# Optimization experiments

Hardware: AMD Instinct MI355X
Metric: run time of the kernel (lower is better)

## Reference

```python
import jax, jax.numpy as jnp
import numpy as np

D_MODEL, H, D_FF = 512, 8, 2048
B, S = 2, 2048
EPS = 1e-6


def _layernorm(x, alpha, beta):
    # Faithful to the torch module: unbiased std (ddof=1), eps added to STD,
    # scalar alpha/beta parameters.
    m = jnp.mean(x, axis=-1, keepdims=True)
    var = jnp.sum((x - m) ** 2, axis=-1, keepdims=True) / (x.shape[-1] - 1)
    std = jnp.sqrt(var)
    return alpha * (x - m) / (std + EPS) + beta


def _mha(x, mask, Wq, bq, Wk, bk, Wv, bv, Wo, bo):
    Bn, Sn, D = x.shape
    dk = D // H
    q = (x @ Wq + bq).reshape(Bn, Sn, H, dk).transpose(0, 2, 1, 3)  # [B,H,S,dk]
    k = (x @ Wk + bk).reshape(Bn, Sn, H, dk).transpose(0, 2, 1, 3)
    v = (x @ Wv + bv).reshape(Bn, Sn, H, dk).transpose(0, 2, 1, 3)
    scores = jnp.einsum('bhqd,bhkd->bhqk', q, k) / jnp.sqrt(jnp.float32(dk))
    scores = jnp.where(mask == 0, -jnp.inf, scores)  # mask [B,1,1,S] broadcasts
    attn = jax.nn.softmax(scores, axis=-1)
    out = jnp.einsum('bhqk,bhkd->bhqd', attn, v)
    out = out.transpose(0, 2, 1, 3).reshape(Bn, Sn, D)
    return out @ Wo + bo


def _ffn(x, W1, b1, W2, b2):
    return jax.nn.relu(x @ W1 + b1) @ W2 + b2


def setup_inputs() -> dict:
    key = jax.random.key(0)
    ks = jax.random.split(key, 12)
    sd = 1.0 / np.sqrt(D_MODEL)
    sdf = 1.0 / np.sqrt(D_FF)
    inp = {
        'x': jax.random.normal(ks[0], (B, S, D_MODEL), jnp.float32),
        'src_mask': jnp.ones((B, 1, 1, S), jnp.int32),
        'Wq': jax.random.normal(ks[1], (D_MODEL, D_MODEL), jnp.float32) * sd,
        'bq': jnp.zeros((D_MODEL,), jnp.float32),
        'Wk': jax.random.normal(ks[2], (D_MODEL, D_MODEL), jnp.float32) * sd,
        'bk': jnp.zeros((D_MODEL,), jnp.float32),
        'Wv': jax.random.normal(ks[3], (D_MODEL, D_MODEL), jnp.float32) * sd,
        'bv': jnp.zeros((D_MODEL,), jnp.float32),
        'Wo': jax.random.normal(ks[4], (D_MODEL, D_MODEL), jnp.float32) * sd,
        'bo': jnp.zeros((D_MODEL,), jnp.float32),
        'W1': jax.random.normal(ks[5], (D_MODEL, D_FF), jnp.float32) * sd,
        'b1': jnp.zeros((D_FF,), jnp.float32),
        'W2': jax.random.normal(ks[6], (D_FF, D_MODEL), jnp.float32) * sdf,
        'b2': jnp.zeros((D_MODEL,), jnp.float32),
        'alpha1': jnp.ones((1,), jnp.float32),
        'beta1': jnp.zeros((1,), jnp.float32),
        'alpha2': jnp.ones((1,), jnp.float32),
        'beta2': jnp.zeros((1,), jnp.float32),
    }
    return inp


def reference(x, src_mask, Wq, bq, Wk, bk, Wv, bv, Wo, bo,
              W1, b1, W2, b2, alpha1, beta1, alpha2, beta2):
    # SkipConnection 0: x + dropout(MHA(LN(x)))  (dropout=0 -> identity)
    h1 = _layernorm(x, alpha1, beta1)
    x = x + _mha(h1, src_mask, Wq, bq, Wk, bk, Wv, bv, Wo, bo)
    # SkipConnection 1: x + dropout(FFN(LN(x)))
    h2 = _layernorm(x, alpha2, beta2)
    x = x + _ffn(h2, W1, b1, W2, b2)
    return x
```

## Files before the change

### kernel.cpp

```cpp
#include <hip/hip_runtime.h>
#include <hip/hip_bf16.h>

typedef __hip_bfloat16 bf16;
typedef __attribute__((ext_vector_type(8))) short s8v;
typedef __attribute__((ext_vector_type(4))) float f32x4;

#define DM 512
#define NH 8
#define DKH 64
#define DFF 2048
#define NB 2
#define NS 2048
#define NR (NB*NS)
#define LN_EPS 1e-6f
#define NEG_BIG (-1e30f)
#define LDQKV (3*DM)
#define SM_SHIFT (-6.0f)
#define PART_ELEMS (NB*NH*NS*DKH)

#define MFMA_B16(a,b,c) __builtin_amdgcn_mfma_f32_16x16x32_bf16(a,b,c,0,0,0)

#define GLOAD16(g, l) __builtin_amdgcn_global_load_lds( \
    (const __attribute__((address_space(1))) void*)(g), \
    (__attribute__((address_space(3))) void*)(l), 16, 0, 0)

__device__ __forceinline__ float us2f(unsigned int u){ return __uint_as_float(u << 16); }
__device__ __forceinline__ float b2f(bf16 v){ return __bfloat162float(v); }
__device__ __forceinline__ float ldf(const float* p){ return *p; }
__device__ __forceinline__ float ldf(const bf16* p){ return __bfloat162float(*p); }
__device__ __forceinline__ void stf(float* p, float v){ *p = v; }
__device__ __forceinline__ void stf(bf16* p, float v){ *p = __float2bfloat16(v); }
__device__ __forceinline__ unsigned short f2bu(float f){
  bf16 b = __float2bfloat16(f);
  return *reinterpret_cast<unsigned short*>(&b);
}

template<int N> __device__ __forceinline__ void waitcnt_vm(){
  if constexpr(N==0)      asm volatile("s_waitcnt vmcnt(0)" ::: "memory");
  else if constexpr(N==2) asm volatile("s_waitcnt vmcnt(2)" ::: "memory");
  else if constexpr(N==3) asm volatile("s_waitcnt vmcnt(3)" ::: "memory");
  else if constexpr(N==4) asm volatile("s_waitcnt vmcnt(4)" ::: "memory");
  else if constexpr(N==6) asm volatile("s_waitcnt vmcnt(6)" ::: "memory");
  else if constexpr(N==8) asm volatile("s_waitcnt vmcnt(8)" ::: "memory");
}

__device__ __forceinline__ int swz(int row, int colbyte){
  return ((row<<7) + colbyte) ^ ((row&7)<<4);
}

__device__ __forceinline__ float wsum(float v){
#pragma unroll
  for(int o=32;o>0;o>>=1) v += __shfl_down(v,o,64);
  return v;
}

template<int NTHR>
__device__ __forceinline__ void stage_tile(char* lds, const bf16* g, int ld, int R, int tid){
  int nch = R*8;
  for(int c = tid; c < nch; c += NTHR){
    int row = c>>3;
    int blk = (c&7) ^ (row&7);
    GLOAD16(g + (size_t)row*ld + blk*8, lds + c*16);
  }
}
__device__ __forceinline__ s8v read_frag(const char* lds, int row, int col){
  return *reinterpret_cast<const s8v*>(lds + swz(row, col<<1));
}

template<typename TI>
__global__ __launch_bounds__(256) void ln_kernel(const TI* __restrict__ x,
    bf16* __restrict__ out, const float* __restrict__ ap, const float* __restrict__ bp){
  __shared__ float s1[4], s2[4];
  int row = blockIdx.x, tid = threadIdx.x;
  const TI* xr = x + (size_t)row*DM;
  float v0 = ldf(xr+tid), v1 = ldf(xr+tid+256);
  float s = wsum(v0+v1);
  float q = wsum(v0*v0+v1*v1);
  int wid = tid>>6, lane = tid&63;
  if(lane==0){ s1[wid]=s; s2[wid]=q; }
  __syncthreads();
  float S = s1[0]+s1[1]+s1[2]+s1[3];
  float Q = s2[0]+s2[1]+s2[2]+s2[3];
  float mean = S*(1.f/DM);
  float var  = (Q - (float)DM*mean*mean)*(1.f/(DM-1));
  float sd   = sqrtf(fmaxf(var,0.f));
  float sc = (*ap)/(sd+LN_EPS);
  float b = *bp;
  bf16* orow = out + (size_t)row*DM;
  orow[tid]     = __float2bfloat16((v0-mean)*sc + b);
  orow[tid+256] = __float2bfloat16((v1-mean)*sc + b);
}

__global__ __launch_bounds__(256) void transpose_all(
    const float* __restrict__ Wq, const float* __restrict__ Wk,
    const float* __restrict__ Wv, const float* __restrict__ Wo,
    const float* __restrict__ W1, const float* __restrict__ W2,
    bf16* __restrict__ WTqkv, bf16* __restrict__ WTo,
    bf16* __restrict__ WT1, bf16* __restrict__ WT2){
  __shared__ float t[64][65];
  int tb = blockIdx.x;
  const float* W; bf16* WT; int K, N, nx;
  if(tb < 192){
    int w = tb>>6; tb &= 63;
    W = (w==0)?Wq:(w==1)?Wk:Wv; WT = WTqkv + w*512*512; K=512; N=512; nx=8;
  } else if(tb < 256){ tb -= 192; W=Wo; WT=WTo; K=512; N=512; nx=8; }
  else if(tb < 512){ tb -= 256; W=W1; WT=WT1; K=512; N=2048; nx=32; }
  else { tb -= 512; W=W2; WT=WT2; K=2048; N=512; nx=8; }
  int n0 = (tb % nx)*64, k0 = (tb / nx)*64;
  int tid = threadIdx.x;
  int rr = tid>>6, cc = tid&63;
#pragma unroll
  for(int r=rr;r<64;r+=4) t[r][cc] = W[(size_t)(k0+r)*N + n0+cc];
  __syncthreads();
#pragma unroll
  for(int r=rr;r<64;r+=4) WT[(size_t)(n0+r)*K + k0+cc] = __float2bfloat16(t[cc][r]);
}

__global__ __launch_bounds__(256) void transpose_v(const bf16* __restrict__ Vg,
    bf16* __restrict__ VT){
  __shared__ float t[64][65];
  int tid = threadIdx.x;
  int s0 = blockIdx.x*64; int bh = blockIdx.y;
  int b = bh>>3, h = bh&7;
  int rr = tid>>6, cc = tid&63;
#pragma unroll
  for(int r=rr;r<64;r+=4)
    t[r][cc] = b2f(Vg[((size_t)(b*NS + s0+r))*LDQKV + h*DKH + cc]);
  __syncthreads();
  int kp = (cc&15)*4 + (cc>>4);
#pragma unroll
  for(int r=rr;r<64;r+=4)
    VT[((size_t)bh*DKH + r)*NS + s0 + kp] = __float2bfloat16(t[cc][r]);
}

template<int BM, int BN, int RELU, int QKVSEL, typename TR, typename TO>
__global__ __launch_bounds__(256) void mfma_gemm(
    const bf16* __restrict__ A, const bf16* __restrict__ WT,
    const float* __restrict__ bias0, const float* __restrict__ bias1,
    const float* __restrict__ bias2,
    const TR* __restrict__ resid, TO* __restrict__ out, int M, int N, int K){
  constexpr int NW = BN/2, NF = NW/16, MI = (BM+31)/32, WRS = BM/2;
  constexpr int LOADS = BM/32 + BN/32;
  __shared__ char lA[2][BM*128];
  __shared__ char lB[2][BN*128];
  int tid = threadIdx.x, wave = tid>>6, lane = tid&63;
  int m0 = blockIdx.x*BM, n0 = blockIdx.y*BN;
  int wr = wave>>1, wc = wave&1;
  int g = lane>>4, li = lane&15;
  f32x4 acc[MI][NF] = {};
  stage_tile<256>(lA[0], A + (size_t)m0*K, K, BM, tid);
  stage_tile<256>(lB[0], WT + (size_t)n0*K, K, BN, tid);
  int NT = K>>6;
  int cur = 0;
  for(int t=0; t<NT; ++t, cur^=1){
    if(t+1 < NT){
      stage_tile<256>(lA[cur^1], A + (size_t)m0*K + (t+1)*64, K, BM, tid);
      stage_tile<256>(lB[cur^1], WT + (size_t)n0*K + (t+1)*64, K, BN, tid);
      waitcnt_vm<LOADS>();
    } else {
      waitcnt_vm<0>();
    }
    __builtin_amdgcn_sched_barrier(0);
    __builtin_amdgcn_s_barrier();
    __builtin_amdgcn_sched_barrier(0);
#pragma unroll
    for(int kk=0; kk<2; kk++){
      s8v af[MI], bfr[NF];
#pragma unroll
      for(int mi=0;mi<MI;mi++) af[mi] = read_frag(lA[cur], wr*WRS+mi*16+li, kk*32+g*8);
#pragma unroll
      for(int ni=0;ni<NF;ni++) bfr[ni] = read_frag(lB[cur], wc*NW+ni*16+li, kk*32+g*8);
#pragma unroll
      for(int mi=0;mi<MI;mi++)
#pragma unroll
        for(int ni=0;ni<NF;ni++)
          acc[mi][ni] = MFMA_B16(af[mi], bfr[ni], acc[mi][ni]);
    }
    __builtin_amdgcn_sched_barrier(0);
    __builtin_amdgcn_s_barrier();
  }
#pragma unroll
  for(int mi=0;mi<MI;mi++)
#pragma unroll
  for(int ni=0;ni<NF;ni++){
    int row = m0 + wr*WRS + mi*16 + g*4;
    int col = n0 + wc*NW + ni*16 + li;
    const float* bp = bias0;
    if(QKVSEL) bp = (col<512)? bias0 : (col<1024)? (bias1-512) : (bias2-1024);
    float bb = bp[col];
#pragma unroll
    for(int r=0;r<4;r++){
      float v = acc[mi][ni][r] + bb;
      if(RELU) v = fmaxf(v, 0.f);
      size_t off = (size_t)(row+r)*N + col;
      if(resid) v += ldf(resid+off);
      stf(out+off, v);
    }
  }
}

__global__ __launch_bounds__(512,4) void flash_attn(
    const bf16* __restrict__ QKV, const bf16* __restrict__ VT,
    const int* __restrict__ mask, bf16* __restrict__ partA,
    bf16* __restrict__ partB, float* __restrict__ lbuf){
  __shared__ char lK[2][64*128];
  __shared__ char lV[2][64*128];
  __shared__ char lP[8][16*128];
  int tid = threadIdx.x, wave = tid>>6, lane = tid&63;
  int bid = blockIdx.x;
  int xcd = bid & 7, u = bid >> 3;
  int q0 = (u & 15)*128;
  int bhk = xcd + 8*(u>>4);
  int h = bhk & 7, kh = (bhk>>3)&1, b = bhk>>4;
  int kbase = kh*(NS/2);
  int g = lane>>4, li = lane&15;
  const bf16* Qg  = QKV + ((size_t)b*NS + q0)*LDQKV + h*DKH;
  const bf16* Kg  = QKV + ((size_t)b*NS + kbase)*LDQKV + DM + h*DKH;
  const bf16* VTg = VT + ((size_t)(b*NH + h))*DKH*NS + kbase;
  stage_tile<512>((char*)lK, Qg, LDQKV, 128, tid);
  __syncthreads();
  s8v qf0 = read_frag((char*)lK, wave*16+li, g*8);
  s8v qf1 = read_frag((char*)lK, wave*16+li, 32+g*8);
  __syncthreads();
  stage_tile<512>(lK[0], Kg, LDQKV, 64, tid);
  stage_tile<512>(lV[0], VTg, NS, 64, tid);
  unsigned long long mb = 0;
#pragma unroll 16
  for(int j=0;j<64;j++)
    mb |= (unsigned long long)(mask[b*NS + kbase + j*16 + li] != 0) << j;
  __syncthreads();
  f32x4 acc[4] = {};
  f32x4 acc_l = {};
  s8v ones;
#pragma unroll
  for(int j=0;j<8;j++) ones[j] = (short)0x3F80;
  char* lPw = lP[wave];

  auto compute = [&](int kt, int c){
    f32x4 S[4] = {};
    __builtin_amdgcn_s_setprio(1);
#pragma unroll
    for(int kk=0;kk<2;kk++){
      s8v qf = kk ? qf1 : qf0;
      s8v kf[4];
#pragma unroll
      for(int ni=0;ni<4;ni++) kf[ni] = read_frag(lK[c], ni*16+li, kk*32+g*8);
#pragma unroll
      for(int ni=0;ni<4;ni++)
        S[ni] = MFMA_B16(qf, kf[ni], S[ni]);
    }
    __builtin_amdgcn_s_setprio(0);
    int jb = kt>>4;
    float madd[4];
#pragma unroll
    for(int ni=0;ni<4;ni++)
      madd[ni] = ((mb>>(jb+ni))&1ull) ? SM_SHIFT : NEG_BIG;
#pragma unroll
    for(int r=0;r<4;r++){
      float e0 = __expf(fmaf(S[0][r], 0.125f, madd[0]));
      float e1 = __expf(fmaf(S[1][r], 0.125f, madd[1]));
      float e2 = __expf(fmaf(S[2][r], 0.125f, madd[2]));
      float e3 = __expf(fmaf(S[3][r], 0.125f, madd[3]));
      int row = g*4 + r;
      uint2 w;
      w.x = (unsigned int)f2bu(e0) | ((unsigned int)f2bu(e1)<<16);
      w.y = (unsigned int)f2bu(e2) | ((unsigned int)f2bu(e3)<<16);
      *reinterpret_cast<uint2*>(lPw + swz(row, li<<3)) = w;
    }
    __builtin_amdgcn_s_setprio(1);
#pragma unroll
    for(int kk=0;kk<2;kk++){
      s8v pf = read_frag(lPw, li, kk*32+g*8);
      s8v vf[4];
#pragma unroll
      for(int nd=0;nd<4;nd++) vf[nd] = read_frag(lV[c], nd*16+li, kk*32+g*8);
#pragma unroll
      for(int nd=0;nd<4;nd++)
        acc[nd] = MFMA_B16(pf, vf[nd], acc[nd]);
      acc_l = MFMA_B16(pf, ones, acc_l);
    }
    __builtin_amdgcn_s_setprio(0);
  };

  int cur = 0;
  for(int t=0; t<15; ++t, cur^=1){
    stage_tile<512>(lK[cur^1], Kg + (size_t)(t+1)*64*LDQKV, LDQKV, 64, tid);
    stage_tile<512>(lV[cur^1], VTg + (t+1)*64, NS, 64, tid);
    waitcnt_vm<2>();
    __builtin_amdgcn_sched_barrier(0);
    __builtin_amdgcn_s_barrier();
    __builtin_amdgcn_sched_barrier(0);
    compute(t*64, cur);
    __builtin_amdgcn_sched_barrier(0);
    __builtin_amdgcn_s_barrier();
  }
  waitcnt_vm<0>();
  __builtin_amdgcn_sched_barrier(0);
  __builtin_amdgcn_s_barrier();
  __builtin_amdgcn_sched_barrier(0);
  compute(15*64, cur);

  bf16* part = kh ? partB : partA;
  size_t qb = (size_t)(b*NH + h)*NS;
#pragma unroll
  for(int r=0;r<4;r++){
    int qrow = q0 + wave*16 + g*4 + r;
#pragma unroll
    for(int nd=0;nd<4;nd++)
      part[(qb + qrow)*DKH + nd*16 + li] = __float2bfloat16(acc[nd][r]);
    if(li==0)
      lbuf[((size_t)((b*NH+h)*2 + kh))*NS + qrow] = acc_l[r];
  }
}

__global__ __launch_bounds__(256) void combine_attn(const bf16* __restrict__ pA,
    const bf16* __restrict__ pB, const float* __restrict__ lbuf,
    bf16* __restrict__ cx){
  int e = blockIdx.x*256 + threadIdx.x;
  int idx = e*4;
  int d = idx & 63, q = (idx>>6)&(NS-1), h = (idx>>17)&7, b = idx>>20;
  uint2 ua = *reinterpret_cast<const uint2*>(pA+idx);
  uint2 ub = *reinterpret_cast<const uint2*>(pB+idx);
  float lA = lbuf[((size_t)((b*NH+h)*2+0))*NS + q];
  float lB = lbuf[((size_t)((b*NH+h)*2+1))*NS + q];
  float il = 1.f/(lA+lB);
  bf16* o = cx + ((size_t)(b*NS+q)*DM + h*DKH + d);
  o[0] = __float2bfloat16((us2f(ua.x&0xffffu)+us2f(ub.x&0xffffu))*il);
  o[1] = __float2bfloat16((us2f(ua.x>>16)+us2f(ub.x>>16))*il);
  o[2] = __float2bfloat16((us2f(ua.y&0xffffu)+us2f(ub.y&0xffffu))*il);
  o[3] = __float2bfloat16((us2f(ua.y>>16)+us2f(ub.y>>16))*il);
}

extern "C" void kernel_launch(void* const* d_in, const int* in_sizes, int n_in,
                              void* d_out, int out_size, void* d_ws, size_t ws_size,
                              hipStream_t stream){
  const float* x   = (const float*)d_in[0];
  const int* mask  = (const int*)d_in[1];
  const float* Wq = (const float*)d_in[2];
  const float* bq = (const float*)d_in[3];
  const float* Wk = (const float*)d_in[4];
  const float* bk = (const float*)d_in[5];
  const float* Wv = (const float*)d_in[6];
  const float* bv = (const float*)d_in[7];
  const float* Wo = (const float*)d_in[8];
  const float* bo = (const float*)d_in[9];
  const float* W1 = (const float*)d_in[10];
  const float* b1 = (const float*)d_in[11];
  const float* W2 = (const float*)d_in[12];
  const float* b2 = (const float*)d_in[13];
  const float* a1 = (const float*)d_in[14];
  const float* be1= (const float*)d_in[15];
  const float* a2 = (const float*)d_in[16];
  const float* be2= (const float*)d_in[17];

  char* ws = (char*)d_ws;
  bf16* h1    = (bf16*)(ws);
  bf16* accA  = (bf16*)(ws);
  bf16* WTqkv = (bf16*)(ws + (size_t)( 4<<20));
  bf16* WTo   = (bf16*)(ws + (size_t)(11<<19));
  bf16* WT1   = (bf16*)(ws + (size_t)( 8<<20));
  bf16* WT2   = (bf16*)(ws + (size_t)(10<<20));
  bf16* qkv   = (bf16*)(ws + (size_t)(12<<20));
  bf16* VT    = (bf16*)(ws + (size_t)(24<<20));
  bf16* cx    = (bf16*)(ws + (size_t)(24<<20));
  bf16* x1    = h1;
  bf16* h2    = (bf16*)(ws + (size_t)( 4<<20));
  bf16* mid   = qkv;
  float* lbuf = (float*)d_out;
  bf16* accB  = (bf16*)((char*)d_out + (1<<20));

  transpose_all<<<768,256,0,stream>>>(Wq,Wk,Wv,Wo,W1,W2, WTqkv,WTo,WT1,WT2);

  ln_kernel<float><<<NR,256,0,stream>>>(x, h1, a1, be1);
  mfma_gemm<128,64,0,1,float,bf16><<<dim3(32,24),256,0,stream>>>(
      h1, WTqkv, bq, bk, bv, (const float*)nullptr, qkv, NR, LDQKV, DM);
  transpose_v<<<dim3(32,16),256,0,stream>>>(qkv + 2*DM, VT);
  flash_attn<<<512,512,0,stream>>>(qkv, VT, mask, accA, accB, lbuf);
  combine_attn<<<PART_ELEMS/1024,256,0,stream>>>(accA, accB, lbuf, cx);
  mfma_gemm<32,64,0,0,float,bf16><<<dim3(128,8),256,0,stream>>>(
      cx, WTo, bo, bo, bo, x, x1, NR, DM, DM);
  ln_kernel<bf16><<<NR,256,0,stream>>>(x1, h2, a2, be2);
  mfma_gemm<128,128,1,0,float,bf16><<<dim3(32,16),256,0,stream>>>(
      h2, WT1, b1, b1, b1, (const float*)nullptr, mid, NR, DFF, DM);
  mfma_gemm<32,64,0,0,bf16,float><<<dim3(128,8),256,0,stream>>>(
      mid, WT2, b2, b2, b2, x1, (float*)d_out, NR, DM, DFF);
}
```

Before: 127.1 us.

## Give each attention wave 32 query rows with 256-thread blocks

The flash attention kernel moves from 8 waves handling 16 query rows each to 4 waves handling 32 rows each, so every K and V fragment read from LDS feeds two MFMA row tiles. Blocks shrink to 256 threads, and the staging and wait counts change to match. This halves the LDS fragment reads per MFMA and the number of waves sharing a barrier. The cost is twice the accumulator registers per wave, fewer threads issuing the global-to-LDS loads, and possibly lower occupancy.

```diff
diff --git a/kernel.cpp b/kernel.cpp
--- a/kernel.cpp
+++ b/kernel.cpp
@@ -199,13 +199,13 @@
   }
 }
 
-__global__ __launch_bounds__(512,4) void flash_attn(
+__global__ __launch_bounds__(256,3) void flash_attn(
     const bf16* __restrict__ QKV, const bf16* __restrict__ VT,
     const int* __restrict__ mask, bf16* __restrict__ partA,
     bf16* __restrict__ partB, float* __restrict__ lbuf){
   __shared__ char lK[2][64*128];
   __shared__ char lV[2][64*128];
-  __shared__ char lP[8][16*128];
+  __shared__ char lP[4][32*128];
   int tid = threadIdx.x, wave = tid>>6, lane = tid&63;
   int bid = blockIdx.x;
   int xcd = bid & 7, u = bid >> 3;
@@ -217,37 +217,42 @@
   const bf16* Qg  = QKV + ((size_t)b*NS + q0)*LDQKV + h*DKH;
   const bf16* Kg  = QKV + ((size_t)b*NS + kbase)*LDQKV + DM + h*DKH;
   const bf16* VTg = VT + ((size_t)(b*NH + h))*DKH*NS + kbase;
-  stage_tile<512>((char*)lK, Qg, LDQKV, 128, tid);
-  __syncthreads();
-  s8v qf0 = read_frag((char*)lK, wave*16+li, g*8);
-  s8v qf1 = read_frag((char*)lK, wave*16+li, 32+g*8);
-  __syncthreads();
-  stage_tile<512>(lK[0], Kg, LDQKV, 64, tid);
-  stage_tile<512>(lV[0], VTg, NS, 64, tid);
+  stage_tile<256>((char*)lK, Qg, LDQKV, 128, tid);
+  __syncthreads();
+  s8v qf[2][2];
+#pragma unroll
+  for(int mi=0;mi<2;mi++)
+#pragma unroll
+    for(int kk=0;kk<2;kk++)
+      qf[mi][kk] = read_frag((char*)lK, wave*32+mi*16+li, kk*32+g*8);
+  __syncthreads();
+  stage_tile<256>(lK[0], Kg, LDQKV, 64, tid);
+  stage_tile<256>(lV[0], VTg, NS, 64, tid);
   unsigned long long mb = 0;
 #pragma unroll 16
   for(int j=0;j<64;j++)
     mb |= (unsigned long long)(mask[b*NS + kbase + j*16 + li] != 0) << j;
   __syncthreads();
-  f32x4 acc[4] = {};
-  f32x4 acc_l = {};
+  f32x4 acc[2][4] = {};
+  f32x4 acc_l[2] = {};
   s8v ones;
 #pragma unroll
   for(int j=0;j<8;j++) ones[j] = (short)0x3F80;
   char* lPw = lP[wave];
 
   auto compute = [&](int kt, int c){
-    f32x4 S[4] = {};
+    f32x4 S[2][4] = {};
     __builtin_amdgcn_s_setprio(1);
 #pragma unroll
     for(int kk=0;kk<2;kk++){
-      s8v qf = kk ? qf1 : qf0;
       s8v kf[4];
 #pragma unroll
       for(int ni=0;ni<4;ni++) kf[ni] = read_frag(lK[c], ni*16+li, kk*32+g*8);
 #pragma unroll
-      for(int ni=0;ni<4;ni++)
-        S[ni] = MFMA_B16(qf, kf[ni], S[ni]);
+      for(int mi=0;mi<2;mi++)
+#pragma unroll
+        for(int ni=0;ni<4;ni++)
+          S[mi][ni] = MFMA_B16(qf[mi][kk], kf[ni], S[mi][ni]);
     }
     __builtin_amdgcn_s_setprio(0);
     int jb = kt>>4;
@@ -256,12 +261,14 @@
     for(int ni=0;ni<4;ni++)
       madd[ni] = ((mb>>(jb+ni))&1ull) ? SM_SHIFT : NEG_BIG;
 #pragma unroll
+    for(int mi=0;mi<2;mi++)
+#pragma unroll
     for(int r=0;r<4;r++){
-      float e0 = __expf(fmaf(S[0][r], 0.125f, madd[0]));
-      float e1 = __expf(fmaf(S[1][r], 0.125f, madd[1]));
-      float e2 = __expf(fmaf(S[2][r], 0.125f, madd[2]));
-      float e3 = __expf(fmaf(S[3][r], 0.125f, madd[3]));
-      int row = g*4 + r;
+      float e0 = __expf(fmaf(S[mi][0][r], 0.125f, madd[0]));
+      float e1 = __expf(fmaf(S[mi][1][r], 0.125f, madd[1]));
+      float e2 = __expf(fmaf(S[mi][2][r], 0.125f, madd[2]));
+      float e3 = __expf(fmaf(S[mi][3][r], 0.125f, madd[3]));
+      int row = mi*16 + g*4 + r;
       uint2 w;
       w.x = (unsigned int)f2bu(e0) | ((unsigned int)f2bu(e1)<<16);
       w.y = (unsigned int)f2bu(e2) | ((unsigned int)f2bu(e3)<<16);
@@ -270,23 +277,26 @@
     __builtin_amdgcn_s_setprio(1);
 #pragma unroll
     for(int kk=0;kk<2;kk++){
-      s8v pf = read_frag(lPw, li, kk*32+g*8);
       s8v vf[4];
 #pragma unroll
       for(int nd=0;nd<4;nd++) vf[nd] = read_frag(lV[c], nd*16+li, kk*32+g*8);
 #pragma unroll
-      for(int nd=0;nd<4;nd++)
-        acc[nd] = MFMA_B16(pf, vf[nd], acc[nd]);
-      acc_l = MFMA_B16(pf, ones, acc_l);
+      for(int mi=0;mi<2;mi++){
+        s8v pf = read_frag(lPw, mi*16+li, kk*32+g*8);
+#pragma unroll
+        for(int nd=0;nd<4;nd++)
+          acc[mi][nd] = MFMA_B16(pf, vf[nd], acc[mi][nd]);
+        acc_l[mi] = MFMA_B16(pf, ones, acc_l[mi]);
+      }
     }
     __builtin_amdgcn_s_setprio(0);
   };
 
   int cur = 0;
   for(int t=0; t<15; ++t, cur^=1){
-    stage_tile<512>(lK[cur^1], Kg + (size_t)(t+1)*64*LDQKV, LDQKV, 64, tid);
-    stage_tile<512>(lV[cur^1], VTg + (t+1)*64, NS, 64, tid);
-    waitcnt_vm<2>();
+    stage_tile<256>(lK[cur^1], Kg + (size_t)(t+1)*64*LDQKV, LDQKV, 64, tid);
+    stage_tile<256>(lV[cur^1], VTg + (t+1)*64, NS, 64, tid);
+    waitcnt_vm<4>();
     __builtin_amdgcn_sched_barrier(0);
     __builtin_amdgcn_s_barrier();
     __builtin_amdgcn_sched_barrier(0);
@@ -303,13 +313,15 @@
   bf16* part = kh ? partB : partA;
   size_t qb = (size_t)(b*NH + h)*NS;
 #pragma unroll
+  for(int mi=0;mi<2;mi++)
+#pragma unroll
   for(int r=0;r<4;r++){
-    int qrow = q0 + wave*16 + g*4 + r;
+    int qrow = q0 + wave*32 + mi*16 + g*4 + r;
 #pragma unroll
     for(int nd=0;nd<4;nd++)
-      part[(qb + qrow)*DKH + nd*16 + li] = __float2bfloat16(acc[nd][r]);
+      part[(qb + qrow)*DKH + nd*16 + li] = __float2bfloat16(acc[mi][nd][r]);
     if(li==0)
-      lbuf[((size_t)((b*NH+h)*2 + kh))*NS + qrow] = acc_l[r];
+      lbuf[((size_t)((b*NH+h)*2 + kh))*NS + qrow] = acc_l[mi][r];
   }
 }
 
@@ -375,7 +387,7 @@
   mfma_gemm<128,64,0,1,float,bf16><<<dim3(32,24),256,0,stream>>>(
       h1, WTqkv, bq, bk, bv, (const float*)nullptr, qkv, NR, LDQKV, DM);
   transpose_v<<<dim3(32,16),256,0,stream>>>(qkv + 2*DM, VT);
-  flash_attn<<<512,512,0,stream>>>(qkv, VT, mask, accA, accB, lbuf);
+  flash_attn<<<512,256,0,stream>>>(qkv, VT, mask, accA, accB, lbuf);
   combine_attn<<<PART_ELEMS/1024,256,0,stream>>>(accA, accB, lbuf, cx);
   mfma_gemm<32,64,0,0,float,bf16><<<dim3(128,8),256,0,stream>>>(
       cx, WTo, bo, bo, bo, x, x1, NR, DM, DM);
```

New measurement: 127.1 us. About the same (+0.0%).

## Fuse weight transpose with first layernorm and double attention key tile size

Applied to the files above, without the earlier changes.

The weight transpose/cast kernel and the first layernorm kernel become one prep kernel, distinguished by block index, which removes one launch and lets the two independent jobs overlap. The flash attention kernel now stages 128 keys per pipeline step (K as one 128-row tile, V as two 64-column halves). That halves the number of loop iterations and block-wide barriers. The cost is LDS per block rising from about 48KB to 80KB, and the launch bound drops from 4 to 2 blocks per CU, so latency hiding may suffer.

```diff
diff --git a/kernel.cpp b/kernel.cpp
--- a/kernel.cpp
+++ b/kernel.cpp
@@ -67,6 +67,55 @@
   return *reinterpret_cast<const s8v*>(lds + swz(row, col<<1));
 }
 
+__global__ __launch_bounds__(256) void prep_kernel(
+    const float* __restrict__ Wq, const float* __restrict__ Wk,
+    const float* __restrict__ Wv, const float* __restrict__ Wo,
+    const float* __restrict__ W1, const float* __restrict__ W2,
+    bf16* __restrict__ WTqkv, bf16* __restrict__ WTo,
+    bf16* __restrict__ WT1, bf16* __restrict__ WT2,
+    const float* __restrict__ x, bf16* __restrict__ h1,
+    const float* __restrict__ ap, const float* __restrict__ bp){
+  __shared__ float t[64][65];
+  __shared__ float s1[4], s2[4];
+  int tid = threadIdx.x;
+  if(blockIdx.x >= 768){
+    int row = blockIdx.x - 768;
+    const float* xr = x + (size_t)row*DM;
+    float v0 = xr[tid], v1 = xr[tid+256];
+    float s = wsum(v0+v1);
+    float q = wsum(v0*v0+v1*v1);
+    int wid = tid>>6, lane = tid&63;
+    if(lane==0){ s1[wid]=s; s2[wid]=q; }
+    __syncthreads();
+    float S = s1[0]+s1[1]+s1[2]+s1[3];
+    float Q = s2[0]+s2[1]+s2[2]+s2[3];
+    float mean = S*(1.f/DM);
+    float var  = (Q - (float)DM*mean*mean)*(1.f/(DM-1));
+    float sd   = sqrtf(fmaxf(var,0.f));
+    float sc = (*ap)/(sd+LN_EPS);
+    float b = *bp;
+    bf16* orow = h1 + (size_t)row*DM;
+    orow[tid]     = __float2bfloat16((v0-mean)*sc + b);
+    orow[tid+256] = __float2bfloat16((v1-mean)*sc + b);
+    return;
+  }
+  int tb = blockIdx.x;
+  const float* W; bf16* WT; int K, N, nx;
+  if(tb < 192){
+    int w = tb>>6; tb &= 63;
+    W = (w==0)?Wq:(w==1)?Wk:Wv; WT = WTqkv + w*512*512; K=512; N=512; nx=8;
+  } else if(tb < 256){ tb -= 192; W=Wo; WT=WTo; K=512; N=512; nx=8; }
+  else if(tb < 512){ tb -= 256; W=W1; WT=WT1; K=512; N=2048; nx=32; }
+  else { tb -= 512; W=W2; WT=WT2; K=2048; N=512; nx=8; }
+  int n0 = (tb % nx)*64, k0 = (tb / nx)*64;
+  int rr = tid>>6, cc = tid&63;
+#pragma unroll
+  for(int r=rr;r<64;r+=4) t[r][cc] = W[(size_t)(k0+r)*N + n0+cc];
+  __syncthreads();
+#pragma unroll
+  for(int r=rr;r<64;r+=4) WT[(size_t)(n0+r)*K + k0+cc] = __float2bfloat16(t[cc][r]);
+}
+
 template<typename TI>
 __global__ __launch_bounds__(256) void ln_kernel(const TI* __restrict__ x,
     bf16* __restrict__ out, const float* __restrict__ ap, const float* __restrict__ bp){
@@ -89,31 +138,6 @@
   bf16* orow = out + (size_t)row*DM;
   orow[tid]     = __float2bfloat16((v0-mean)*sc + b);
   orow[tid+256] = __float2bfloat16((v1-mean)*sc + b);
-}
-
-__global__ __launch_bounds__(256) void transpose_all(
-    const float* __restrict__ Wq, const float* __restrict__ Wk,
-    const float* __restrict__ Wv, const float* __restrict__ Wo,
-    const float* __restrict__ W1, const float* __restrict__ W2,
-    bf16* __restrict__ WTqkv, bf16* __restrict__ WTo,
-    bf16* __restrict__ WT1, bf16* __restrict__ WT2){
-  __shared__ float t[64][65];
-  int tb = blockIdx.x;
-  const float* W; bf16* WT; int K, N, nx;
-  if(tb < 192){
-    int w = tb>>6; tb &= 63;
-    W = (w==0)?Wq:(w==1)?Wk:Wv; WT = WTqkv + w*512*512; K=512; N=512; nx=8;
-  } else if(tb < 256){ tb -= 192; W=Wo; WT=WTo; K=512; N=512; nx=8; }
-  else if(tb < 512){ tb -= 256; W=W1; WT=WT1; K=512; N=2048; nx=32; }
-  else { tb -= 512; W=W2; WT=WT2; K=2048; N=512; nx=8; }
-  int n0 = (tb % nx)*64, k0 = (tb / nx)*64;
-  int tid = threadIdx.x;
-  int rr = tid>>6, cc = tid&63;
-#pragma unroll
-  for(int r=rr;r<64;r+=4) t[r][cc] = W[(size_t)(k0+r)*N + n0+cc];
-  __syncthreads();
-#pragma unroll
-  for(int r=rr;r<64;r+=4) WT[(size_t)(n0+r)*K + k0+cc] = __float2bfloat16(t[cc][r]);
 }
 
 __global__ __launch_bounds__(256) void transpose_v(const bf16* __restrict__ Vg,
@@ -199,12 +223,12 @@
   }
 }
 
-__global__ __launch_bounds__(512,4) void flash_attn(
+__global__ __launch_bounds__(512,2) void flash_attn(
     const bf16* __restrict__ QKV, const bf16* __restrict__ VT,
     const int* __restrict__ mask, bf16* __restrict__ partA,
     bf16* __restrict__ partB, float* __restrict__ lbuf){
-  __shared__ char lK[2][64*128];
-  __shared__ char lV[2][64*128];
+  __shared__ char lK[2][128*128];
+  __shared__ char lV[2][2][64*128];
   __shared__ char lP[8][16*128];
   int tid = threadIdx.x, wave = tid>>6, lane = tid&63;
   int bid = blockIdx.x;
@@ -217,13 +241,14 @@
   const bf16* Qg  = QKV + ((size_t)b*NS + q0)*LDQKV + h*DKH;
   const bf16* Kg  = QKV + ((size_t)b*NS + kbase)*LDQKV + DM + h*DKH;
   const bf16* VTg = VT + ((size_t)(b*NH + h))*DKH*NS + kbase;
-  stage_tile<512>((char*)lK, Qg, LDQKV, 128, tid);
-  __syncthreads();
-  s8v qf0 = read_frag((char*)lK, wave*16+li, g*8);
-  s8v qf1 = read_frag((char*)lK, wave*16+li, 32+g*8);
-  __syncthreads();
-  stage_tile<512>(lK[0], Kg, LDQKV, 64, tid);
-  stage_tile<512>(lV[0], VTg, NS, 64, tid);
+  stage_tile<512>(lK[0], Qg, LDQKV, 128, tid);
+  __syncthreads();
+  s8v qf0 = read_frag(lK[0], wave*16+li, g*8);
+  s8v qf1 = read_frag(lK[0], wave*16+li, 32+g*8);
+  __syncthreads();
+  stage_tile<512>(lK[0], Kg, LDQKV, 128, tid);
+  stage_tile<512>(lV[0][0], VTg,      NS, 64, tid);
+  stage_tile<512>(lV[0][1], VTg + 64, NS, 64, tid);
   unsigned long long mb = 0;
 #pragma unroll 16
   for(int j=0;j<64;j++)
@@ -236,61 +261,65 @@
   for(int j=0;j<8;j++) ones[j] = (short)0x3F80;
   char* lPw = lP[wave];
 
-  auto compute = [&](int kt, int c){
-    f32x4 S[4] = {};
-    __builtin_amdgcn_s_setprio(1);
-#pragma unroll
-    for(int kk=0;kk<2;kk++){
-      s8v qf = kk ? qf1 : qf0;
-      s8v kf[4];
-#pragma unroll
-      for(int ni=0;ni<4;ni++) kf[ni] = read_frag(lK[c], ni*16+li, kk*32+g*8);
+  auto compute = [&](int t, int c){
+#pragma unroll
+    for(int s=0;s<2;s++){
+      f32x4 S[4] = {};
+      __builtin_amdgcn_s_setprio(1);
+#pragma unroll
+      for(int kk=0;kk<2;kk++){
+        s8v qf = kk ? qf1 : qf0;
+        s8v kf[4];
+#pragma unroll
+        for(int ni=0;ni<4;ni++) kf[ni] = read_frag(lK[c], s*64+ni*16+li, kk*32+g*8);
+#pragma unroll
+        for(int ni=0;ni<4;ni++)
+          S[ni] = MFMA_B16(qf, kf[ni], S[ni]);
+      }
+      __builtin_amdgcn_s_setprio(0);
+      int jb = t*8 + s*4;
+      float madd[4];
 #pragma unroll
       for(int ni=0;ni<4;ni++)
-        S[ni] = MFMA_B16(qf, kf[ni], S[ni]);
+        madd[ni] = ((mb>>(jb+ni))&1ull) ? SM_SHIFT : NEG_BIG;
+#pragma unroll
+      for(int r=0;r<4;r++){
+        float e0 = __expf(fmaf(S[0][r], 0.125f, madd[0]));
+        float e1 = __expf(fmaf(S[1][r], 0.125f, madd[1]));
+        float e2 = __expf(fmaf(S[2][r], 0.125f, madd[2]));
+        float e3 = __expf(fmaf(S[3][r], 0.125f, madd[3]));
+        int row = g*4 + r;
+        uint2 w;
+        w.x = (unsigned int)f2bu(e0) | ((unsigned int)f2bu(e1)<<16);
+        w.y = (unsigned int)f2bu(e2) | ((unsigned int)f2bu(e3)<<16);
+        *reinterpret_cast<uint2*>(lPw + swz(row, li<<3)) = w;
+      }
+      __builtin_amdgcn_s_setprio(1);
+#pragma unroll
+      for(int kk=0;kk<2;kk++){
+        s8v pf = read_frag(lPw, li, kk*32+g*8);
+        s8v vf[4];
+#pragma unroll
+        for(int nd=0;nd<4;nd++) vf[nd] = read_frag(lV[c][s], nd*16+li, kk*32+g*8);
+#pragma unroll
+        for(int nd=0;nd<4;nd++)
+          acc[nd] = MFMA_B16(pf, vf[nd], acc[nd]);
+        acc_l = MFMA_B16(pf, ones, acc_l);
+      }
+      __builtin_amdgcn_s_setprio(0);
     }
-    __builtin_amdgcn_s_setprio(0);
-    int jb = kt>>4;
-    float madd[4];
-#pragma unroll
-    for(int ni=0;ni<4;ni++)
-      madd[ni] = ((mb>>(jb+ni))&1ull) ? SM_SHIFT : NEG_BIG;
-#pragma unroll
-    for(int r=0;r<4;r++){
-      float e0 = __expf(fmaf(S[0][r], 0.125f, madd[0]));
-      float e1 = __expf(fmaf(S[1][r], 0.125f, madd[1]));
-      float e2 = __expf(fmaf(S[2][r], 0.125f, madd[2]));
-      float e3 = __expf(fmaf(S[3][r], 0.125f, madd[3]));
-      int row = g*4 + r;
-      uint2 w;
-      w.x = (unsigned int)f2bu(e0) | ((unsigned int)f2bu(e1)<<16);
-      w.y = (unsigned int)f2bu(e2) | ((unsigned int)f2bu(e3)<<16);
-      *reinterpret_cast<uint2*>(lPw + swz(row, li<<3)) = w;
-    }
-    __builtin_amdgcn_s_setprio(1);
-#pragma unroll
-    for(int kk=0;kk<2;kk++){
-      s8v pf = read_frag(lPw, li, kk*32+g*8);
-      s8v vf[4];
-#pragma unroll
-      for(int nd=0;nd<4;nd++) vf[nd] = read_frag(lV[c], nd*16+li, kk*32+g*8);
-#pragma unroll
-      for(int nd=0;nd<4;nd++)
-        acc[nd] = MFMA_B16(pf, vf[nd], acc[nd]);
-      acc_l = MFMA_B16(pf, ones, acc_l);
-    }
-    __builtin_amdgcn_s_setprio(0);
   };
 
   int cur = 0;
-  for(int t=0; t<15; ++t, cur^=1){
-    stage_tile<512>(lK[cur^1], Kg + (size_t)(t+1)*64*LDQKV, LDQKV, 64, tid);
-    stage_tile<512>(lV[cur^1], VTg + (t+1)*64, NS, 64, tid);
-    waitcnt_vm<2>();
+  for(int t=0; t<7; ++t, cur^=1){
+    stage_tile<512>(lK[cur^1], Kg + (size_t)(t+1)*128*LDQKV, LDQKV, 128, tid);
+    stage_tile<512>(lV[cur^1][0], VTg + (t+1)*128,      NS, 64, tid);
+    stage_tile<512>(lV[cur^1][1], VTg + (t+1)*128 + 64, NS, 64, tid);
+    waitcnt_vm<4>();
     __builtin_amdgcn_sched_barrier(0);
     __builtin_amdgcn_s_barrier();
     __builtin_amdgcn_sched_barrier(0);
-    compute(t*64, cur);
+    compute(t, cur);
     __builtin_amdgcn_sched_barrier(0);
     __builtin_amdgcn_s_barrier();
   }
@@ -298,7 +327,7 @@
   __builtin_amdgcn_sched_barrier(0);
   __builtin_amdgcn_s_barrier();
   __builtin_amdgcn_sched_barrier(0);
-  compute(15*64, cur);
+  compute(7, cur);
 
   bf16* part = kh ? partB : partA;
   size_t qb = (size_t)(b*NH + h)*NS;
@@ -369,9 +398,8 @@
   float* lbuf = (float*)d_out;
   bf16* accB  = (bf16*)((char*)d_out + (1<<20));
 
-  transpose_all<<<768,256,0,stream>>>(Wq,Wk,Wv,Wo,W1,W2, WTqkv,WTo,WT1,WT2);
-
-  ln_kernel<float><<<NR,256,0,stream>>>(x, h1, a1, be1);
+  prep_kernel<<<4864,256,0,stream>>>(Wq,Wk,Wv,Wo,W1,W2, WTqkv,WTo,WT1,WT2,
+                                     x, h1, a1, be1);
   mfma_gemm<128,64,0,1,float,bf16><<<dim3(32,24),256,0,stream>>>(
       h1, WTqkv, bq, bk, bv, (const float*)nullptr, qkv, NR, LDQKV, DM);
   transpose_v<<<dim3(32,16),256,0,stream>>>(qkv + 2*DM, VT);
```

Result: faster. 121.5 us (-4.4%).
